# Kernel optimization log

Hardware: AMD Instinct MI355X
Metric: run time of the kernel (lower is better)

The kernel has to match this reference:

```python
import jax, jax.numpy as jnp
import numpy as np

ALPHA = 2.0
B, C, H, W = 4, 2, 256, 256
_INF = 1e9  # larger than any squared pixel distance (max ~ (H+W)^2)


def _dt1d(f):
    # exact 1D squared distance transform via brute-force min-convolution
    # d[i] = min_j f[j] + (i-j)^2, vectorized along the last axis
    n = f.shape[-1]
    i = jnp.arange(n, dtype=f.dtype)
    d2 = (i[:, None] - i[None, :]) ** 2  # [n_out, n_in]
    return jnp.min(f[..., None, :] + d2, axis=-1)


def _edt(mask):
    # scipy.ndimage.distance_transform_edt semantics:
    # distance from each nonzero (True) element to the nearest zero (False) element
    f = jnp.where(mask, jnp.float32(_INF), jnp.float32(0.0))
    f = _dt1d(f)  # pass along W
    f = jnp.swapaxes(_dt1d(jnp.swapaxes(f, -1, -2)), -1, -2)  # pass along H
    return jnp.sqrt(f)


def _distance_field(img):
    # img: (B, 1, H, W) float; field = edt(fg) + edt(bg), zeroed when no fg (matches fg_mask.any() guard)
    fg = img > 0.5
    field = _edt(fg) + _edt(~fg)
    has_fg = jnp.any(fg, axis=(1, 2, 3), keepdims=True)
    return jnp.where(has_fg, field, jnp.float32(0.0))


def setup_inputs() -> dict:
    key = jax.random.key(0)
    k1, k2 = jax.random.split(key)
    model_output = jax.random.normal(k1, (B, C, H, W), dtype=jnp.float32)
    ground_truth = (jax.random.uniform(k2, (B, 1, H, W)) > 0.5).astype(jnp.float32)
    return {"model_output": model_output, "ground_truth": ground_truth}


def reference(model_output, ground_truth):
    # argmax over channel dim -> binary label map (b, 1, H, W)
    pred = jnp.argmax(model_output, axis=1)[:, None, :, :].astype(jnp.float32)
    pred_dt = _distance_field(pred)
    gt_dt = _distance_field(ground_truth)
    # original detaches the error term (no_grad loss)
    err = jax.lax.stop_gradient((pred - ground_truth) ** 2)
    dist = pred_dt ** ALPHA + gt_dt ** ALPHA
    return jnp.mean(err * dist)
```

## Files before the change

### kernel.cpp

```cpp
#include <hip/hip_runtime.h>

#define NSIDE 256
#define HW    65536
#define NB    4
#define NMAP  8

static const size_t D1_OFF    = 0;
static const size_t ROWFG_OFF = (size_t)NMAP * HW * 4;
static const size_t PART_OFF  = ROWFG_OFF + (size_t)NMAP * NSIDE;

__device__ __forceinline__ int nearest_bit(const unsigned long long* z, int x) {
    int xw = x >> 6, xb = x & 63;
    int best = 1 << 20;
    unsigned long long w = z[xw] & ((2ull << xb) - 1ull);
    if (w) {
        best = x - ((xw << 6) + 63 - __clzll(w));
    } else {
        for (int k = xw - 1; k >= 0; --k) {
            if (z[k]) { best = x - ((k << 6) + 63 - __clzll(z[k])); break; }
        }
    }
    unsigned long long w2 = z[xw] & (~0ull << xb);
    if (w2) {
        int r = (xw << 6) + __builtin_ctzll(w2);
        if (r - x < best) best = r - x;
    } else {
        for (int k = xw + 1; k < 4; ++k) {
            if (z[k]) {
                int r = (k << 6) + __builtin_ctzll(z[k]);
                if (r - x < best) best = r - x;
                break;
            }
        }
    }
    return best;
}

__global__ void k_rowmask(const float* __restrict__ mo, const float* __restrict__ gt,
                          unsigned int* __restrict__ d1p, unsigned char* __restrict__ rowFg) {
    int m = blockIdx.x >> 8;
    int y = blockIdx.x & 255;
    int x = threadIdx.x;
    int bit;
    if (m < NB) {
        float c0 = mo[(size_t)(m * 2 + 0) * HW + y * NSIDE + x];
        float c1 = mo[(size_t)(m * 2 + 1) * HW + y * NSIDE + x];
        bit = (c1 > c0) ? 1 : 0;
    } else {
        bit = (gt[(size_t)(m - NB) * HW + y * NSIDE + x] > 0.5f) ? 1 : 0;
    }
    __shared__ unsigned long long zF[4], zB[4];
    unsigned long long balF = __ballot(bit == 0);
    unsigned long long balB = __ballot(bit != 0);
    if ((threadIdx.x & 63) == 0) {
        zF[threadIdx.x >> 6] = balF;
        zB[threadIdx.x >> 6] = balB;
    }
    __syncthreads();
    int dF = nearest_bit(zF, x);
    int dB = nearest_bit(zB, x);
    unsigned int vF = (dF > 255) ? 0xFFFFu : (unsigned int)(dF * dF);
    unsigned int vB = (dB > 255) ? 0xFFFFu : (unsigned int)(dB * dB);
    d1p[((size_t)m * NSIDE + x) * NSIDE + y] = vF | (vB << 16);
    if (threadIdx.x == 0)
        rowFg[m * NSIDE + y] = ((zB[0] | zB[1] | zB[2] | zB[3]) != 0ull) ? 1 : 0;
}

__global__ void k_colreduce(const unsigned int* __restrict__ d1p,
                            float* __restrict__ part) {
    int b = blockIdx.x >> 8;
    int x = blockIdx.x & 255;
    int y = threadIdx.x;
    __shared__ float cPf[NSIDE], cPb[NSIDE], cGf[NSIDE], cGb[NSIDE];
    unsigned int P = d1p[((size_t)b * NSIDE + x) * NSIDE + y];
    unsigned int G = d1p[((size_t)(NB + b) * NSIDE + x) * NSIDE + y];
    unsigned int pf = P & 0xFFFFu, pb = P >> 16;
    unsigned int gf = G & 0xFFFFu, gb = G >> 16;
    cPf[y] = (pf == 0xFFFFu) ? 1e9f : (float)pf;
    cPb[y] = (pb == 0xFFFFu) ? 1e9f : (float)pb;
    cGf[y] = (gf == 0xFFFFu) ? 1e9f : (float)gf;
    cGb[y] = (gb == 0xFFFFu) ? 1e9f : (float)gb;
    __syncthreads();
    float e = ((pf != 0u) != (gf != 0u)) ? 1.0f : 0.0f;
    float bPf = cPf[y], bPb = cPb[y], bGf = cGf[y], bGb = cGb[y];
    if (e == 0.0f) { bPf = 0.0f; bPb = 0.0f; bGf = 0.0f; bGb = 0.0f; }
    float fr = 0.0f;
    for (int r = 1; r < NSIDE; ++r) {
        fr += 1.0f;
        float drr = fr * fr;
        float bmax = fmaxf(fmaxf(bPf, bPb), fmaxf(bGf, bGb));
        if (__all(drr >= bmax)) break;
        int jm = y - r, jp = y + r;
        int jmc = jm < 0 ? 0 : jm;
        int jpc = jp > (NSIDE - 1) ? (NSIDE - 1) : jp;
        float aPf = cPf[jmc], aPb = cPb[jmc], aGf = cGf[jmc], aGb = cGb[jmc];
        float qPf = cPf[jpc], qPb = cPb[jpc], qGf = cGf[jpc], qGb = cGb[jpc];
        if (jm < 0) { aPf = 3e9f; aPb = 3e9f; aGf = 3e9f; aGb = 3e9f; }
        if (jp > NSIDE - 1) { qPf = 3e9f; qPb = 3e9f; qGf = 3e9f; qGb = 3e9f; }
        bPf = fminf(bPf, fminf(aPf, qPf) + drr);
        bPb = fminf(bPb, fminf(aPb, qPb) + drr);
        bGf = fminf(bGf, fminf(aGf, qGf) + drr);
        bGb = fminf(bGb, fminf(aGb, qGb) + drr);
    }
    float sP = e * (bPf + bPb);
    float sG = e * (bGf + bGb);
#pragma unroll
    for (int off = 32; off > 0; off >>= 1) {
        sP += __shfl_down(sP, off, 64);
        sG += __shfl_down(sG, off, 64);
    }
    __shared__ float rP[4], rG[4];
    int wid = threadIdx.x >> 6;
    if ((threadIdx.x & 63) == 0) { rP[wid] = sP; rG[wid] = sG; }
    __syncthreads();
    if (threadIdx.x == 0) {
        part[b * NSIDE + x]        = rP[0] + rP[1] + rP[2] + rP[3];
        part[(NB + b) * NSIDE + x] = rG[0] + rG[1] + rG[2] + rG[3];
    }
}

__global__ void k_final(const unsigned char* __restrict__ rowFg,
                        const float* __restrict__ part,
                        float* __restrict__ out) {
    int tid = threadIdx.x;
    int lane = tid & 63, w = tid >> 6;
    __shared__ int hasFg[NMAP];
    __shared__ float red[NMAP];
    if (tid < NMAP) hasFg[tid] = 0;
    __syncthreads();
    unsigned long long v = ((const unsigned long long*)rowFg)[tid];
    if (v) atomicOr(&hasFg[tid >> 5], 1);
#pragma unroll
    for (int k = 0; k < 2; ++k) {
        int m = 2 * w + k;
        float4 f = ((const float4*)part)[m * 64 + lane];
        float s = f.x + f.y + f.z + f.w;
#pragma unroll
        for (int off = 32; off > 0; off >>= 1) s += __shfl_down(s, off, 64);
        if (lane == 0) red[m] = s;
    }
    __syncthreads();
    if (tid == 0) {
        double t = 0.0;
#pragma unroll
        for (int m = 0; m < NMAP; ++m)
            if (hasFg[m]) t += (double)red[m];
        out[0] = (float)(t * (1.0 / (double)(NB * HW)));
    }
}

extern "C" void kernel_launch(void* const* d_in, const int* in_sizes, int n_in,
                              void* d_out, int out_size, void* d_ws, size_t ws_size,
                              hipStream_t stream) {
    const float* mo = (const float*)d_in[0];
    const float* gt = (const float*)d_in[1];
    float* out = (float*)d_out;
    char* ws = (char*)d_ws;

    unsigned int* d1p    = (unsigned int*)(ws + D1_OFF);
    unsigned char* rowFg = (unsigned char*)(ws + ROWFG_OFF);
    float* part          = (float*)(ws + PART_OFF);

    hipLaunchKernelGGL(k_rowmask,   dim3(NMAP * 256), dim3(256), 0, stream, mo, gt, d1p, rowFg);
    hipLaunchKernelGGL(k_colreduce, dim3(NB * 256),   dim3(256), 0, stream, d1p, part);
    hipLaunchKernelGGL(k_final,     dim3(1),          dim3(256), 0, stream, rowFg, part, out);
}
```

Before: 66.35 us.

## Process 16 rows per block in row pass and write transposed output as uint4

The row pass now gives each block 16 consecutive rows instead of one. It stores their ballot masks in shared memory, then each thread computes 16 results for its column and writes them as four 16-byte vector stores to the transposed buffer. This replaces scattered 4-byte strided stores with contiguous vector writes. In exchange the grid shrinks from 2048 to 128 blocks, which lowers parallelism and the latency hiding available for the loads, and each thread holds 16 results in registers.

```diff
diff --git a/kernel.cpp b/kernel.cpp
--- a/kernel.cpp
+++ b/kernel.cpp
@@ -36,34 +36,52 @@
     return best;
 }
 
-__global__ void k_rowmask(const float* __restrict__ mo, const float* __restrict__ gt,
-                          unsigned int* __restrict__ d1p, unsigned char* __restrict__ rowFg) {
-    int m = blockIdx.x >> 8;
-    int y = blockIdx.x & 255;
+__global__ void k_rowdt(const float* __restrict__ mo, const float* __restrict__ gt,
+                        unsigned int* __restrict__ d1p, unsigned char* __restrict__ rowFg) {
+    int m = blockIdx.x >> 4;
+    int g = blockIdx.x & 15;
     int x = threadIdx.x;
-    int bit;
-    if (m < NB) {
-        float c0 = mo[(size_t)(m * 2 + 0) * HW + y * NSIDE + x];
-        float c1 = mo[(size_t)(m * 2 + 1) * HW + y * NSIDE + x];
-        bit = (c1 > c0) ? 1 : 0;
-    } else {
-        bit = (gt[(size_t)(m - NB) * HW + y * NSIDE + x] > 0.5f) ? 1 : 0;
-    }
-    __shared__ unsigned long long zF[4], zB[4];
-    unsigned long long balF = __ballot(bit == 0);
-    unsigned long long balB = __ballot(bit != 0);
-    if ((threadIdx.x & 63) == 0) {
-        zF[threadIdx.x >> 6] = balF;
-        zB[threadIdx.x >> 6] = balB;
+    int y0 = g * 16;
+    __shared__ unsigned long long zF[16][4], zB[16][4];
+
+    for (int r = 0; r < 16; ++r) {
+        int y = y0 + r;
+        int bit;
+        if (m < NB) {
+            float c0 = mo[(size_t)(m * 2 + 0) * HW + y * NSIDE + x];
+            float c1 = mo[(size_t)(m * 2 + 1) * HW + y * NSIDE + x];
+            bit = (c1 > c0) ? 1 : 0;
+        } else {
+            bit = (gt[(size_t)(m - NB) * HW + y * NSIDE + x] > 0.5f) ? 1 : 0;
+        }
+        unsigned long long balF = __ballot(bit == 0);
+        unsigned long long balB = __ballot(bit != 0);
+        if ((x & 63) == 0) {
+            zF[r][x >> 6] = balF;
+            zB[r][x >> 6] = balB;
+        }
     }
     __syncthreads();
-    int dF = nearest_bit(zF, x);
-    int dB = nearest_bit(zB, x);
-    unsigned int vF = (dF > 255) ? 0xFFFFu : (unsigned int)(dF * dF);
-    unsigned int vB = (dB > 255) ? 0xFFFFu : (unsigned int)(dB * dB);
-    d1p[((size_t)m * NSIDE + x) * NSIDE + y] = vF | (vB << 16);
-    if (threadIdx.x == 0)
-        rowFg[m * NSIDE + y] = ((zB[0] | zB[1] | zB[2] | zB[3]) != 0ull) ? 1 : 0;
+
+    unsigned int res[16];
+#pragma unroll
+    for (int r = 0; r < 16; ++r) {
+        int dF = nearest_bit(zF[r], x);
+        int dB = nearest_bit(zB[r], x);
+        unsigned int vF = (dF > 255) ? 0xFFFFu : (unsigned int)(dF * dF);
+        unsigned int vB = (dB > 255) ? 0xFFFFu : (unsigned int)(dB * dB);
+        res[r] = vF | (vB << 16);
+    }
+    unsigned int* dst = &d1p[((size_t)m * NSIDE + x) * NSIDE + y0];
+    uint4* dst4 = (uint4*)dst;
+#pragma unroll
+    for (int q = 0; q < 4; ++q)
+        dst4[q] = make_uint4(res[q * 4 + 0], res[q * 4 + 1], res[q * 4 + 2], res[q * 4 + 3]);
+    if (x < 16) {
+        int r = x;
+        rowFg[m * NSIDE + y0 + r] =
+            ((zB[r][0] | zB[r][1] | zB[r][2] | zB[r][3]) != 0ull) ? 1 : 0;
+    }
 }
 
 __global__ void k_colreduce(const unsigned int* __restrict__ d1p,
@@ -161,7 +179,7 @@
     unsigned char* rowFg = (unsigned char*)(ws + ROWFG_OFF);
     float* part          = (float*)(ws + PART_OFF);
 
-    hipLaunchKernelGGL(k_rowmask,   dim3(NMAP * 256), dim3(256), 0, stream, mo, gt, d1p, rowFg);
-    hipLaunchKernelGGL(k_colreduce, dim3(NB * 256),   dim3(256), 0, stream, d1p, part);
-    hipLaunchKernelGGL(k_final,     dim3(1),          dim3(256), 0, stream, rowFg, part, out);
+    hipLaunchKernelGGL(k_rowdt,     dim3(NMAP * 16), dim3(256), 0, stream, mo, gt, d1p, rowFg);
+    hipLaunchKernelGGL(k_colreduce, dim3(NB * 256),  dim3(256), 0, stream, d1p, part);
+    hipLaunchKernelGGL(k_final,     dim3(1),         dim3(256), 0, stream, rowFg, part, out);
 }
```

New measurement: 73.90 us. +11.4%, slower.

## Store packed row bitmasks and compute 1D row distances inside column kernel

Applied to the files above, without the earlier changes.

The first kernel now writes only four 64-bit ballot masks per row instead of a transposed 32-bit packed distance map, which cuts its global writes from 2 MB to 64 KB and drops the strided transposed store. The column kernel reloads those masks, which every thread in a block reads the same way because they are small and cached. It recomputes each row's nearest-zero and nearest-one distances with branchless clz/ctz over the four words. This trades memory traffic for extra integer ALU work in the column pass.

```diff
diff --git a/kernel.cpp b/kernel.cpp
--- a/kernel.cpp
+++ b/kernel.cpp
@@ -5,39 +5,14 @@
 #define NB    4
 #define NMAP  8
 
-static const size_t D1_OFF    = 0;
-static const size_t ROWFG_OFF = (size_t)NMAP * HW * 4;
+typedef unsigned long long u64;
+
+static const size_t ZZ_OFF    = 0;
+static const size_t ROWFG_OFF = (size_t)NMAP * NSIDE * 4 * 8;
 static const size_t PART_OFF  = ROWFG_OFF + (size_t)NMAP * NSIDE;
 
-__device__ __forceinline__ int nearest_bit(const unsigned long long* z, int x) {
-    int xw = x >> 6, xb = x & 63;
-    int best = 1 << 20;
-    unsigned long long w = z[xw] & ((2ull << xb) - 1ull);
-    if (w) {
-        best = x - ((xw << 6) + 63 - __clzll(w));
-    } else {
-        for (int k = xw - 1; k >= 0; --k) {
-            if (z[k]) { best = x - ((k << 6) + 63 - __clzll(z[k])); break; }
-        }
-    }
-    unsigned long long w2 = z[xw] & (~0ull << xb);
-    if (w2) {
-        int r = (xw << 6) + __builtin_ctzll(w2);
-        if (r - x < best) best = r - x;
-    } else {
-        for (int k = xw + 1; k < 4; ++k) {
-            if (z[k]) {
-                int r = (k << 6) + __builtin_ctzll(z[k]);
-                if (r - x < best) best = r - x;
-                break;
-            }
-        }
-    }
-    return best;
-}
-
-__global__ void k_rowmask(const float* __restrict__ mo, const float* __restrict__ gt,
-                          unsigned int* __restrict__ d1p, unsigned char* __restrict__ rowFg) {
+__global__ void k_bits(const float* __restrict__ mo, const float* __restrict__ gt,
+                       u64* __restrict__ zz, unsigned char* __restrict__ rowFg) {
     int m = blockIdx.x >> 8;
     int y = blockIdx.x & 255;
     int x = threadIdx.x;
@@ -49,39 +24,69 @@
     } else {
         bit = (gt[(size_t)(m - NB) * HW + y * NSIDE + x] > 0.5f) ? 1 : 0;
     }
-    __shared__ unsigned long long zF[4], zB[4];
-    unsigned long long balF = __ballot(bit == 0);
-    unsigned long long balB = __ballot(bit != 0);
-    if ((threadIdx.x & 63) == 0) {
-        zF[threadIdx.x >> 6] = balF;
-        zB[threadIdx.x >> 6] = balB;
+    u64 fg = __ballot(bit);
+    __shared__ u64 s[4];
+    int wid = x >> 6;
+    if ((x & 63) == 0) {
+        zz[((size_t)m * NSIDE + y) * 4 + wid] = fg;
+        s[wid] = fg;
     }
     __syncthreads();
-    int dF = nearest_bit(zF, x);
-    int dB = nearest_bit(zB, x);
-    unsigned int vF = (dF > 255) ? 0xFFFFu : (unsigned int)(dF * dF);
-    unsigned int vB = (dB > 255) ? 0xFFFFu : (unsigned int)(dB * dB);
-    d1p[((size_t)m * NSIDE + x) * NSIDE + y] = vF | (vB << 16);
-    if (threadIdx.x == 0)
-        rowFg[m * NSIDE + y] = ((zB[0] | zB[1] | zB[2] | zB[3]) != 0ull) ? 1 : 0;
+    if (x == 0)
+        rowFg[m * NSIDE + y] = ((s[0] | s[1] | s[2] | s[3]) != 0ull) ? 1 : 0;
 }
 
-__global__ void k_colreduce(const unsigned int* __restrict__ d1p,
-                            float* __restrict__ part) {
+__device__ __forceinline__ int nbit(u64 z0, u64 z1, u64 z2, u64 z3,
+                                    int xw, u64 loM, u64 hiM, int x) {
+    u64 a0 = (xw == 0) ? (z0 & loM) : z0;
+    u64 a1 = (xw < 1) ? 0ull : ((xw == 1) ? (z1 & loM) : z1);
+    u64 a2 = (xw < 2) ? 0ull : ((xw == 2) ? (z2 & loM) : z2);
+    u64 a3 = (xw < 3) ? 0ull : ((xw == 3) ? (z3 & loM) : z3);
+    int msb = -(1 << 20);
+    msb = a0 ? (63  - __builtin_clzll(a0)) : msb;
+    msb = a1 ? (127 - __builtin_clzll(a1)) : msb;
+    msb = a2 ? (191 - __builtin_clzll(a2)) : msb;
+    msb = a3 ? (255 - __builtin_clzll(a3)) : msb;
+    int dl = x - msb;
+    u64 b0 = (xw > 0) ? 0ull : (z0 & hiM);
+    u64 b1 = (xw > 1) ? 0ull : ((xw == 1) ? (z1 & hiM) : z1);
+    u64 b2 = (xw > 2) ? 0ull : ((xw == 2) ? (z2 & hiM) : z2);
+    u64 b3 = (xw == 3) ? (z3 & hiM) : z3;
+    int lsb = 1 << 20;
+    lsb = b3 ? (192 + __builtin_ctzll(b3)) : lsb;
+    lsb = b2 ? (128 + __builtin_ctzll(b2)) : lsb;
+    lsb = b1 ? (64  + __builtin_ctzll(b1)) : lsb;
+    lsb = b0 ? (      __builtin_ctzll(b0)) : lsb;
+    int dr = lsb - x;
+    return dl < dr ? dl : dr;
+}
+
+__global__ void k_colreduce(const u64* __restrict__ zz, float* __restrict__ part) {
     int b = blockIdx.x >> 8;
     int x = blockIdx.x & 255;
     int y = threadIdx.x;
+    const u64* zp = &zz[((size_t)b * NSIDE + y) * 4];
+    const u64* zg = &zz[((size_t)(NB + b) * NSIDE + y) * 4];
+    u64 p0 = zp[0], p1 = zp[1], p2 = zp[2], p3 = zp[3];
+    u64 g0 = zg[0], g1 = zg[1], g2 = zg[2], g3 = zg[3];
+    int xw = x >> 6, xb = x & 63;
+    u64 loM = (2ull << xb) - 1ull;
+    u64 hiM = ~0ull << xb;
+    int dPf = nbit(~p0, ~p1, ~p2, ~p3, xw, loM, hiM, x);
+    int dPb = nbit( p0,  p1,  p2,  p3, xw, loM, hiM, x);
+    int dGf = nbit(~g0, ~g1, ~g2, ~g3, xw, loM, hiM, x);
+    int dGb = nbit( g0,  g1,  g2,  g3, xw, loM, hiM, x);
     __shared__ float cPf[NSIDE], cPb[NSIDE], cGf[NSIDE], cGb[NSIDE];
-    unsigned int P = d1p[((size_t)b * NSIDE + x) * NSIDE + y];
-    unsigned int G = d1p[((size_t)(NB + b) * NSIDE + x) * NSIDE + y];
-    unsigned int pf = P & 0xFFFFu, pb = P >> 16;
-    unsigned int gf = G & 0xFFFFu, gb = G >> 16;
-    cPf[y] = (pf == 0xFFFFu) ? 1e9f : (float)pf;
-    cPb[y] = (pb == 0xFFFFu) ? 1e9f : (float)pb;
-    cGf[y] = (gf == 0xFFFFu) ? 1e9f : (float)gf;
-    cGb[y] = (gb == 0xFFFFu) ? 1e9f : (float)gb;
+    cPf[y] = (dPf > 255) ? 1e9f : (float)(dPf * dPf);
+    cPb[y] = (dPb > 255) ? 1e9f : (float)(dPb * dPb);
+    cGf[y] = (dGf > 255) ? 1e9f : (float)(dGf * dGf);
+    cGb[y] = (dGb > 255) ? 1e9f : (float)(dGb * dGb);
     __syncthreads();
-    float e = ((pf != 0u) != (gf != 0u)) ? 1.0f : 0.0f;
+    u64 pw = (xw == 0) ? p0 : (xw == 1) ? p1 : (xw == 2) ? p2 : p3;
+    u64 gw = (xw == 0) ? g0 : (xw == 1) ? g1 : (xw == 2) ? g2 : g3;
+    int predBit = (int)((pw >> xb) & 1ull);
+    int gtBit   = (int)((gw >> xb) & 1ull);
+    float e = (predBit != gtBit) ? 1.0f : 0.0f;
     float bPf = cPf[y], bPb = cPb[y], bGf = cGf[y], bGb = cGb[y];
     if (e == 0.0f) { bPf = 0.0f; bPb = 0.0f; bGf = 0.0f; bGb = 0.0f; }
     float fr = 0.0f;
@@ -128,7 +133,7 @@
     __shared__ float red[NMAP];
     if (tid < NMAP) hasFg[tid] = 0;
     __syncthreads();
-    unsigned long long v = ((const unsigned long long*)rowFg)[tid];
+    u64 v = ((const u64*)rowFg)[tid];
     if (v) atomicOr(&hasFg[tid >> 5], 1);
 #pragma unroll
     for (int k = 0; k < 2; ++k) {
@@ -157,11 +162,11 @@
     float* out = (float*)d_out;
     char* ws = (char*)d_ws;
 
-    unsigned int* d1p    = (unsigned int*)(ws + D1_OFF);
+    u64* zz              = (u64*)(ws + ZZ_OFF);
     unsigned char* rowFg = (unsigned char*)(ws + ROWFG_OFF);
     float* part          = (float*)(ws + PART_OFF);
 
-    hipLaunchKernelGGL(k_rowmask,   dim3(NMAP * 256), dim3(256), 0, stream, mo, gt, d1p, rowFg);
-    hipLaunchKernelGGL(k_colreduce, dim3(NB * 256),   dim3(256), 0, stream, d1p, part);
+    hipLaunchKernelGGL(k_bits,      dim3(NMAP * 256), dim3(256), 0, stream, mo, gt, zz, rowFg);
+    hipLaunchKernelGGL(k_colreduce, dim3(NB * 256),   dim3(256), 0, stream, zz, part);
     hipLaunchKernelGGL(k_final,     dim3(1),          dim3(256), 0, stream, rowFg, part, out);
 }
```

New measurement: 64.62 us. -2.6%, faster.
